# Performance work log

Measured on AMD Instinct MI355X. Metric: run time of the kernel, lower is better.

Reference implementation:

```python
import jax, jax.numpy as jnp
import numpy as np

K, D = 4096, 256
BETA, DECAY, EPS = 0.25, 0.99, 1e-05
B = 32768


def setup_inputs() -> dict:
    key = jax.random.key(0)
    k1, k2, k3, k4 = jax.random.split(key, 4)
    return {
        "z_e": jax.random.normal(k1, (B, D), dtype=jnp.float32),
        "codebook": jax.random.normal(k2, (K, D), dtype=jnp.float32),
        "ema_cluster_size": jax.random.uniform(k3, (K,), dtype=jnp.float32),
        "ema_weight": jax.random.normal(k4, (K, D), dtype=jnp.float32),
    }


def reference(z_e, codebook, ema_cluster_size, ema_weight):
    z_e = z_e.astype(jnp.float32)
    # squared L2 distances: ||z||^2 - 2 z.C^T + ||C||^2  (chunking in torch is
    # purely a memory optimization; math is identical)
    e_norm = jnp.sum(z_e * z_e, axis=1, keepdims=True)            # [B,1]
    c_norm = jnp.sum(codebook * codebook, axis=1)                  # [K]
    dists = e_norm - 2.0 * (z_e @ codebook.T) + c_norm[None, :]    # [B,K]
    idx = jnp.argmin(dists, axis=1)                                # [B] int

    z_q = codebook[idx]                                            # [B,d] gather

    # EMA codebook update (no_grad in torch)
    counts = jnp.zeros((K,), jnp.float32).at[idx].add(1.0)         # bincount
    new_cluster = ema_cluster_size * DECAY + counts * (1.0 - DECAY)
    dw = jnp.zeros((K, D), jnp.float32).at[idx].add(z_e)           # index_add_
    new_ema_weight = ema_weight * DECAY + dw * (1.0 - DECAY)
    n = jnp.sum(new_cluster)
    cluster_size = (new_cluster + EPS) / (n + K * EPS) * n
    new_codebook = new_ema_weight / cluster_size[:, None]

    z_q_ste = z_e + jax.lax.stop_gradient(z_q - z_e)
    commit = BETA * jnp.mean((z_e - z_q) ** 2)
    return (z_q_ste, idx, commit, new_codebook, new_cluster, new_ema_weight)
```

## Files before the change

kernel.cpp:

```cpp
#include <hip/hip_runtime.h>

#define KC 4096
#define DD 256
#define BB 32768
#define P_BETA 0.25f
#define P_DECAY 0.99f
#define P_EPS 1e-5f
#define TAU 0.5f
#define CHUNK 16

typedef __attribute__((ext_vector_type(8))) short bf16x8;
typedef __attribute__((ext_vector_type(4))) float f32x4;

static __device__ __forceinline__ unsigned short f2bf(float f) {
    unsigned int u = __float_as_uint(f);
    unsigned int r = (u + 0x7fffu + ((u >> 16) & 1u)) >> 16;
    return (unsigned short)r;
}
static __device__ __forceinline__ void gload_lds16(const void* g, void* s) {
    __builtin_amdgcn_global_load_lds(
        (const __attribute__((address_space(1))) unsigned int*)g,
        (__attribute__((address_space(3))) unsigned int*)s, 16, 0, 0);
}

#define ZBLK (BB * DD / 4 / 256)
#define CBLK (KC * DD / 4 / 256)
#define EBLK (KC * DD / 4 / 256)
__global__ __launch_bounds__(256) void convert_all_kernel(
    const float* __restrict__ z, const float* __restrict__ cb,
    unsigned short* __restrict__ zb, unsigned short* __restrict__ cbb,
    float* __restrict__ cn, int* __restrict__ cnt,
    const float* __restrict__ ema_w, float* __restrict__ out_emaw) {
    const int b = blockIdx.x;
    if (b < ZBLK) {
        int t = b * 256 + threadIdx.x;
        float4 v = ((const float4*)z)[t];
        *(ushort4*)&zb[(size_t)t * 4] =
            make_ushort4(f2bf(v.x), f2bf(v.y), f2bf(v.z), f2bf(v.w));
    } else if (b < ZBLK + CBLK) {
        int t = (b - ZBLK) * 256 + threadIdx.x;
        int lane = threadIdx.x & 63;
        int row = (b - ZBLK) * 4 + (threadIdx.x >> 6);
        float4 v = ((const float4*)cb)[t];
        *(ushort4*)&cbb[(size_t)t * 4] =
            make_ushort4(f2bf(v.x), f2bf(v.y), f2bf(v.z), f2bf(v.w));
        float s = v.x * v.x + v.y * v.y + v.z * v.z + v.w * v.w;
#pragma unroll
        for (int m = 32; m; m >>= 1) s += __shfl_xor(s, m);
        if (lane == 0) cn[row] = s;
    } else if (b == ZBLK + CBLK) {
        int4* p = (int4*)cnt;
        int4 zv = make_int4(0, 0, 0, 0);
#pragma unroll
        for (int j = 0; j < 4; ++j) p[threadIdx.x * 4 + j] = zv;
    } else {
        int t = (b - ZBLK - CBLK - 1) * 256 + threadIdx.x;
        float4 v = ((const float4*)ema_w)[t];
        ((float4*)out_emaw)[t] =
            make_float4(v.x * P_DECAY, v.y * P_DECAY, v.z * P_DECAY, v.w * P_DECAY);
    }
}

__global__ __launch_bounds__(256, 2) void
mfma_argmin_kernel(const unsigned short* __restrict__ zb,
                   const unsigned short* __restrict__ cbb,
                   const float* __restrict__ cn,
                   float4* __restrict__ cand) {
    __shared__ unsigned short As[128 * 256];
    __shared__ unsigned short Bs[128 * 64];

    const int tid = threadIdx.x;
    const int l = tid & 63, w = tid >> 6;
    const int xcd = blockIdx.x & 7;
    const int half = xcd >> 2;
    const int rb = (blockIdx.x >> 3) * 4 + (xcd & 3);
    const int row0 = rb * 128;
    const int col0 = half * 2048;
    const int wm = w & 1, wn = w >> 1;
    const int m_off = wm * 64, n_off = wn * 64;
    const int lm = l & 15, lq = l >> 4;

    {
        const int lrow = w * 2 + (l >> 5);
        const int coff = ((l & 31) ^ lrow) * 8;
#pragma unroll
        for (int i = 0; i < 16; ++i) {
            gload_lds16(zb + (size_t)(row0 + i * 8 + lrow) * DD + coff,
                        &As[(i * 8 + w * 2) * 256]);
        }
    }

    const int srow = l >> 3;
    const int scol = ((l & 7) ^ srow) * 8;
    const int g0 = w * 4;

    float best[16];
    int bidx[16];
#pragma unroll
    for (int s = 0; s < 16; ++s) { best[s] = 3.4e38f; bidx[s] = 0; }

    for (int kc = 0; kc < 2048; kc += 128) {
        f32x4 acc[4][4];
#pragma unroll
        for (int a = 0; a < 4; ++a)
#pragma unroll
            for (int b = 0; b < 4; ++b) acc[a][b] = (f32x4){0.f, 0.f, 0.f, 0.f};

        for (int dc = 0; dc < 4; ++dc) {
#pragma unroll
            for (int j = 0; j < 4; ++j) {
                const int g = g0 + j;
                const int br = col0 + kc + g * 8 + srow;
                gload_lds16(cbb + (size_t)br * DD + dc * 64 + scol, &Bs[g * 512]);
            }
            __syncthreads();
#pragma unroll
            for (int ks = 0; ks < 2; ++ks) {
                bf16x8 af[4], bfr[4];
                const int cbi = dc * 8 + ks * 4 + lq;
#pragma unroll
                for (int tm = 0; tm < 4; ++tm) {
                    int r = m_off + tm * 16 + lm;
                    af[tm] = *(const bf16x8*)&As[r * 256 + ((cbi ^ (r & 7)) * 8)];
                }
#pragma unroll
                for (int tn = 0; tn < 4; ++tn) {
                    int r = n_off + tn * 16 + lm;
                    bfr[tn] = *(const bf16x8*)&Bs[r * 64 + (((ks * 4 + lq) ^ (r & 7)) * 8)];
                }
#pragma unroll
                for (int tm = 0; tm < 4; ++tm)
#pragma unroll
                    for (int tn = 0; tn < 4; ++tn)
                        acc[tm][tn] = __builtin_amdgcn_mfma_f32_16x16x32_bf16(
                            af[tm], bfr[tn], acc[tm][tn], 0, 0, 0);
            }
            __syncthreads();
        }
#pragma unroll
        for (int tn = 0; tn < 4; ++tn) {
            const int col = col0 + kc + n_off + tn * 16 + lm;
            const float cnv = cn[col];
#pragma unroll
            for (int tm = 0; tm < 4; ++tm)
#pragma unroll
                for (int r = 0; r < 4; ++r) {
                    float dist = fmaf(-2.0f, acc[tm][tn][r], cnv);
                    int s = tm * 4 + r;
                    if (dist < best[s]) { best[s] = dist; bidx[s] = col; }
                }
        }
    }

    float v2[16];
    int i2[16];
#pragma unroll
    for (int s = 0; s < 16; ++s) { v2[s] = 3.4e38f; i2[s] = 0x7fffffff; }
#pragma unroll
    for (int m = 1; m < 16; m <<= 1) {
#pragma unroll
        for (int s = 0; s < 16; ++s) {
            float w1 = __shfl_xor(best[s], m); int j1 = __shfl_xor(bidx[s], m);
            float w2 = __shfl_xor(v2[s], m);   int j2 = __shfl_xor(i2[s], m);
            bool b = (w1 < best[s]) || (w1 == best[s] && j1 < bidx[s]);
            if (b) {
                bool c = (best[s] < w2) || (best[s] == w2 && bidx[s] < j2);
                v2[s] = c ? best[s] : w2; i2[s] = c ? bidx[s] : j2;
                best[s] = w1; bidx[s] = j1;
            } else {
                bool c = (w1 < v2[s]) || (w1 == v2[s] && j1 < i2[s]);
                v2[s] = c ? w1 : v2[s]; i2[s] = c ? j1 : i2[s];
            }
        }
    }

    float4* red = (float4*)As;
    if (lm == 0) {
#pragma unroll
        for (int tm = 0; tm < 4; ++tm)
#pragma unroll
            for (int r = 0; r < 4; ++r) {
                int s = tm * 4 + r;
                int row_local = m_off + tm * 16 + lq * 4 + r;
                red[wn * 128 + row_local] =
                    make_float4(best[s], __int_as_float(bidx[s]), v2[s], __int_as_float(i2[s]));
            }
    }
    __syncthreads();
    if (tid < 128) {
        float4 a = red[tid], b = red[128 + tid];
        float av1 = a.x, av2 = a.z; int ai1 = __float_as_int(a.y), ai2 = __float_as_int(a.w);
        float bv1 = b.x, bv2 = b.z; int bi1 = __float_as_int(b.y), bi2 = __float_as_int(b.w);
        float v1o, v2o; int i1o, i2o;
        bool bb = (bv1 < av1) || (bv1 == av1 && bi1 < ai1);
        if (bb) {
            v1o = bv1; i1o = bi1;
            bool c = (av1 < bv2) || (av1 == bv2 && ai1 < bi2);
            v2o = c ? av1 : bv2; i2o = c ? ai1 : bi2;
        } else {
            v1o = av1; i1o = ai1;
            bool c = (bv1 < av2) || (bv1 == av2 && bi1 < ai2);
            v2o = c ? bv1 : av2; i2o = c ? bi1 : ai2;
        }
        cand[(size_t)half * BB + row0 + tid] =
            make_float4(v1o, __int_as_float(i1o), v2o, __int_as_float(i2o));
    }
}

__global__ __launch_bounds__(256) void merge_refine_kernel(
    const float4* __restrict__ cand, const float* __restrict__ z,
    const float* __restrict__ cb, const float* __restrict__ cn,
    int* __restrict__ idx_i, float* __restrict__ idx_f,
    int* __restrict__ cnt) {
    const int w = threadIdx.x >> 6, l = threadIdx.x & 63;
    const int i = blockIdx.x * 4 + w;
    float4 a = cand[i], b = cand[(size_t)BB + i];
    float av1 = a.x, av2 = a.z; int ai1 = __float_as_int(a.y), ai2 = __float_as_int(a.w);
    float bv1 = b.x, bv2 = b.z; int bi1 = __float_as_int(b.y), bi2 = __float_as_int(b.w);
    float v1o, v2o; int i1o, i2o;
    bool bb = (bv1 < av1) || (bv1 == av1 && bi1 < ai1);
    if (bb) {
        v1o = bv1; i1o = bi1;
        bool c = (av1 < bv2) || (av1 == bv2 && ai1 < bi2);
        v2o = c ? av1 : bv2; i2o = c ? ai1 : bi2;
    } else {
        v1o = av1; i1o = ai1;
        bool c = (bv1 < av2) || (bv1 == av2 && bi1 < ai2);
        v2o = c ? bv1 : av2; i2o = c ? bi1 : ai2;
    }
    int kb = i1o;
    if (v2o - v1o < TAU) {
        float4 zv = ((const float4*)z)[(size_t)i * 64 + l];
        float4 p = ((const float4*)cb)[(size_t)i1o * 64 + l];
        float4 q = ((const float4*)cb)[(size_t)i2o * 64 + l];
        float s1 = zv.x * p.x + zv.y * p.y + zv.z * p.z + zv.w * p.w;
        float s2 = zv.x * q.x + zv.y * q.y + zv.z * q.z + zv.w * q.w;
#pragma unroll
        for (int m = 32; m; m >>= 1) {
            s1 += __shfl_xor(s1, m);
            s2 += __shfl_xor(s2, m);
        }
        float d1 = cn[i1o] - 2.f * s1;
        float d2 = cn[i2o] - 2.f * s2;
        if (d2 < d1 || (d2 == d1 && i2o < i1o)) kb = i2o;
    }
    if (l == 0) {
        idx_i[i] = kb;
        idx_f[i] = (float)kb;
        atomicAdd(&cnt[kb], 1);
    }
}

__global__ __launch_bounds__(256) void prefix_kernel(
    const int* __restrict__ cnt, int* __restrict__ cursor,
    const float* __restrict__ ema_cs, float* __restrict__ out_cluster,
    float* __restrict__ n_ws) {
    __shared__ int ls[257];
    __shared__ float lns[4];
    const int t = threadIdx.x;
    int local[16];
    int s = 0;
    float ns = 0.f;
#pragma unroll
    for (int j = 0; j < 16; ++j) {
        int c = cnt[t * 16 + j];
        local[j] = s; s += c;
        float nc = ema_cs[t * 16 + j] * P_DECAY + (float)c * (1.0f - P_DECAY);
        out_cluster[t * 16 + j] = nc;
        ns += nc;
    }
    ls[t + 1] = s;
#pragma unroll
    for (int m = 32; m; m >>= 1) ns += __shfl_xor(ns, m);
    if ((t & 63) == 0) lns[t >> 6] = ns;
    __syncthreads();
    if (t == 0) {
        ls[0] = 0;
        for (int j = 1; j <= 256; ++j) ls[j] += ls[j - 1];
        *n_ws = lns[0] + lns[1] + lns[2] + lns[3];
    }
    __syncthreads();
    int off = ls[t];
#pragma unroll
    for (int j = 0; j < 16; ++j) cursor[t * 16 + j] = off + local[j];
}

__global__ __launch_bounds__(256) void zq_commit_scatter_kernel(
    const float* __restrict__ z, const float* __restrict__ cb,
    const int* __restrict__ idx_i, float* __restrict__ zq,
    float* __restrict__ commit_parts, int* __restrict__ cursor,
    int* __restrict__ row_of) {
    const int w = threadIdx.x >> 6, l = threadIdx.x & 63;
    const int i = blockIdx.x * 4 + w;
    const int k = idx_i[i];
    float4 zv = ((const float4*)z)[(size_t)i * 64 + l];
    float4 cv = ((const float4*)cb)[(size_t)k * 64 + l];
    ((float4*)zq)[(size_t)i * 64 + l] = cv;
    float dx = zv.x - cv.x, dy = zv.y - cv.y, dz = zv.z - cv.z, dq = zv.w - cv.w;
    float s = dx * dx + dy * dy + dz * dz + dq * dq;
#pragma unroll
    for (int m = 32; m; m >>= 1) s += __shfl_xor(s, m);
    __shared__ float ls[4];
    if (l == 0) {
        ls[w] = s;
        int pos = atomicAdd(&cursor[k], 1);
        row_of[pos] = i | (k << 16);
    }
    __syncthreads();
    if (threadIdx.x == 0) commit_parts[blockIdx.x] = ls[0] + ls[1] + ls[2] + ls[3];
}

__global__ __launch_bounds__(256) void bucket_scatter_kernel(
    const float* __restrict__ z, const int* __restrict__ row_of,
    float* __restrict__ out_emaw, const float* __restrict__ commit_parts,
    float* __restrict__ out_commit) {
    const int t = threadIdx.x;
    if (blockIdx.x == BB / CHUNK) {
        float cs = 0.f;
        for (int j = t; j < BB / 4; j += 256) cs += commit_parts[j];
#pragma unroll
        for (int m = 32; m; m >>= 1) cs += __shfl_xor(cs, m);
        __shared__ float lc[4];
        if ((t & 63) == 0) lc[t >> 6] = cs;
        __syncthreads();
        if (t == 0)
            *out_commit = P_BETA * (lc[0] + lc[1] + lc[2] + lc[3]) / (float)((size_t)BB * DD);
        return;
    }
    __shared__ int pk[CHUNK];
    const int p0 = blockIdx.x * CHUNK;
    if (t < CHUNK) pk[t] = row_of[p0 + t];
    __syncthreads();
    float acc = 0.f;
    int kprev = pk[0] >> 16;
#pragma unroll 4
    for (int j = 0; j < CHUNK; ++j) {
        int p = pk[j];
        int r = p & 0xffff, k = p >> 16;
        if (k != kprev) {
            atomicAdd(&out_emaw[(size_t)kprev * DD + t], acc * (1.0f - P_DECAY));
            acc = 0.f;
            kprev = k;
        }
        acc += z[(size_t)r * DD + t];
    }
    atomicAdd(&out_emaw[(size_t)kprev * DD + t], acc * (1.0f - P_DECAY));
}

__global__ __launch_bounds__(256) void codebook_kernel(
    const float* __restrict__ out_emaw, const float* __restrict__ out_cluster,
    const float* __restrict__ n_ws, float* __restrict__ out_codebook) {
    const int id4 = blockIdx.x * 256 + threadIdx.x;
    const int k = id4 >> 6;
    const float n = *n_ws;
    float4 v = ((const float4*)out_emaw)[id4];
    float cl = out_cluster[k];
    float inv = 1.0f / ((cl + P_EPS) / (n + (float)KC * P_EPS) * n);
    ((float4*)out_codebook)[id4] =
        make_float4(v.x * inv, v.y * inv, v.z * inv, v.w * inv);
}

extern "C" void kernel_launch(void* const* d_in, const int* in_sizes, int n_in,
                              void* d_out, int out_size, void* d_ws, size_t ws_size,
                              hipStream_t stream) {
    const float* z      = (const float*)d_in[0];
    const float* cb     = (const float*)d_in[1];
    const float* ema_cs = (const float*)d_in[2];
    const float* ema_w  = (const float*)d_in[3];

    float4* cand = (float4*)d_ws;
    unsigned short* zb = (unsigned short*)(cand + 2 * (size_t)BB);
    unsigned short* cbb = zb + (size_t)BB * DD;
    float* c_norm = (float*)(cbb + (size_t)KC * DD);
    int* idx_i = (int*)(c_norm + KC);
    int* cnt = idx_i + BB;
    int* cursor = cnt + KC;
    int* row_of = cursor + KC;
    float* commit_parts = (float*)(row_of + BB);
    float* n_ws = commit_parts + BB / 4;

    float* out        = (float*)d_out;
    float* o_zq       = out;
    float* o_idx      = o_zq + (size_t)BB * DD;
    float* o_commit   = o_idx + BB;
    float* o_codebook = o_commit + 1;
    float* o_cluster  = o_codebook + (size_t)KC * DD;
    float* o_emaw     = o_cluster + KC;

    convert_all_kernel<<<ZBLK + CBLK + 1 + EBLK, 256, 0, stream>>>(
        z, cb, zb, cbb, c_norm, cnt, ema_w, o_emaw);
    mfma_argmin_kernel<<<(BB / 128) * 2, 256, 0, stream>>>(zb, cbb, c_norm, cand);
    merge_refine_kernel<<<BB / 4, 256, 0, stream>>>(cand, z, cb, c_norm, idx_i,
                                                    o_idx, cnt);
    prefix_kernel<<<1, 256, 0, stream>>>(cnt, cursor, ema_cs, o_cluster, n_ws);
    zq_commit_scatter_kernel<<<BB / 4, 256, 0, stream>>>(z, cb, idx_i, o_zq,
                                                         commit_parts, cursor, row_of);
    bucket_scatter_kernel<<<BB / CHUNK + 1, 256, 0, stream>>>(
        z, row_of, o_emaw, commit_parts, o_commit);
    codebook_kernel<<<(KC * DD / 4) / 256, 256, 0, stream>>>(
        o_emaw, o_cluster, n_ws, o_codebook);
    (void)in_sizes; (void)n_in; (void)out_size; (void)ws_size;
}
```

Baseline: 228.1 us.

## Fuse merge, zq, commit and direct atomic EMA scatter; drop bucket sort

Merges the candidate-merge/refine, z_q gather, commit partial and EMA weight accumulation into one kernel that adds z rows directly into the EMA weights with per-element atomics. This removes the prefix sort, bucket scatter and separate codebook kernels. The finalize kernel has every block recompute the cluster sum n redundantly. In exchange, 32768×256 float atomics go to global memory, which may contend on popular codes, and the floating-point summation order becomes nondeterministic.

```diff
diff --git a/kernel.cpp b/kernel.cpp
--- a/kernel.cpp
+++ b/kernel.cpp
@@ -7,7 +7,6 @@
 #define P_DECAY 0.99f
 #define P_EPS 1e-5f
 #define TAU 0.5f
-#define CHUNK 16
 
 typedef __attribute__((ext_vector_type(8))) short bf16x8;
 typedef __attribute__((ext_vector_type(4))) float f32x4;
@@ -207,11 +206,12 @@
     }
 }
 
-__global__ __launch_bounds__(256) void merge_refine_kernel(
+__global__ __launch_bounds__(256) void merge_zq_kernel(
     const float4* __restrict__ cand, const float* __restrict__ z,
     const float* __restrict__ cb, const float* __restrict__ cn,
-    int* __restrict__ idx_i, float* __restrict__ idx_f,
-    int* __restrict__ cnt) {
+    float* __restrict__ idx_f, int* __restrict__ cnt,
+    float* __restrict__ zq, float* __restrict__ commit_parts,
+    float* __restrict__ out_emaw) {
     const int w = threadIdx.x >> 6, l = threadIdx.x & 63;
     const int i = blockIdx.x * 4 + w;
     float4 a = cand[i], b = cand[(size_t)BB + i];
@@ -228,10 +228,11 @@
         bool c = (bv1 < av2) || (bv1 == av2 && bi1 < ai2);
         v2o = c ? bv1 : av2; i2o = c ? bi1 : ai2;
     }
+    float4 zv = ((const float4*)z)[(size_t)i * 64 + l];
+    float4 p = ((const float4*)cb)[(size_t)i1o * 64 + l];
     int kb = i1o;
+    float4 cv = p;
     if (v2o - v1o < TAU) {
-        float4 zv = ((const float4*)z)[(size_t)i * 64 + l];
-        float4 p = ((const float4*)cb)[(size_t)i1o * 64 + l];
         float4 q = ((const float4*)cb)[(size_t)i2o * 64 + l];
         float s1 = zv.x * p.x + zv.y * p.y + zv.z * p.z + zv.w * p.w;
         float s2 = zv.x * q.x + zv.y * q.y + zv.z * q.z + zv.w * q.w;
@@ -242,80 +243,36 @@
         }
         float d1 = cn[i1o] - 2.f * s1;
         float d2 = cn[i2o] - 2.f * s2;
-        if (d2 < d1 || (d2 == d1 && i2o < i1o)) kb = i2o;
-    }
-    if (l == 0) {
-        idx_i[i] = kb;
-        idx_f[i] = (float)kb;
-        atomicAdd(&cnt[kb], 1);
-    }
-}
-
-__global__ __launch_bounds__(256) void prefix_kernel(
-    const int* __restrict__ cnt, int* __restrict__ cursor,
-    const float* __restrict__ ema_cs, float* __restrict__ out_cluster,
-    float* __restrict__ n_ws) {
-    __shared__ int ls[257];
-    __shared__ float lns[4];
-    const int t = threadIdx.x;
-    int local[16];
-    int s = 0;
-    float ns = 0.f;
-#pragma unroll
-    for (int j = 0; j < 16; ++j) {
-        int c = cnt[t * 16 + j];
-        local[j] = s; s += c;
-        float nc = ema_cs[t * 16 + j] * P_DECAY + (float)c * (1.0f - P_DECAY);
-        out_cluster[t * 16 + j] = nc;
-        ns += nc;
-    }
-    ls[t + 1] = s;
-#pragma unroll
-    for (int m = 32; m; m >>= 1) ns += __shfl_xor(ns, m);
-    if ((t & 63) == 0) lns[t >> 6] = ns;
-    __syncthreads();
-    if (t == 0) {
-        ls[0] = 0;
-        for (int j = 1; j <= 256; ++j) ls[j] += ls[j - 1];
-        *n_ws = lns[0] + lns[1] + lns[2] + lns[3];
-    }
-    __syncthreads();
-    int off = ls[t];
-#pragma unroll
-    for (int j = 0; j < 16; ++j) cursor[t * 16 + j] = off + local[j];
-}
-
-__global__ __launch_bounds__(256) void zq_commit_scatter_kernel(
-    const float* __restrict__ z, const float* __restrict__ cb,
-    const int* __restrict__ idx_i, float* __restrict__ zq,
-    float* __restrict__ commit_parts, int* __restrict__ cursor,
-    int* __restrict__ row_of) {
-    const int w = threadIdx.x >> 6, l = threadIdx.x & 63;
-    const int i = blockIdx.x * 4 + w;
-    const int k = idx_i[i];
-    float4 zv = ((const float4*)z)[(size_t)i * 64 + l];
-    float4 cv = ((const float4*)cb)[(size_t)k * 64 + l];
+        if (d2 < d1 || (d2 == d1 && i2o < i1o)) { kb = i2o; cv = q; }
+    }
     ((float4*)zq)[(size_t)i * 64 + l] = cv;
     float dx = zv.x - cv.x, dy = zv.y - cv.y, dz = zv.z - cv.z, dq = zv.w - cv.w;
     float s = dx * dx + dy * dy + dz * dz + dq * dq;
 #pragma unroll
     for (int m = 32; m; m >>= 1) s += __shfl_xor(s, m);
+    const float sc = 1.0f - P_DECAY;
+    float* dst = out_emaw + (size_t)kb * DD + l * 4;
+    atomicAdd(dst + 0, zv.x * sc);
+    atomicAdd(dst + 1, zv.y * sc);
+    atomicAdd(dst + 2, zv.z * sc);
+    atomicAdd(dst + 3, zv.w * sc);
     __shared__ float ls[4];
     if (l == 0) {
         ls[w] = s;
-        int pos = atomicAdd(&cursor[k], 1);
-        row_of[pos] = i | (k << 16);
+        idx_f[i] = (float)kb;
+        atomicAdd(&cnt[kb], 1);
     }
     __syncthreads();
     if (threadIdx.x == 0) commit_parts[blockIdx.x] = ls[0] + ls[1] + ls[2] + ls[3];
 }
 
-__global__ __launch_bounds__(256) void bucket_scatter_kernel(
-    const float* __restrict__ z, const int* __restrict__ row_of,
-    float* __restrict__ out_emaw, const float* __restrict__ commit_parts,
+__global__ __launch_bounds__(256) void finalize_kernel(
+    const int* __restrict__ cnt, const float* __restrict__ ema_cs,
+    const float* __restrict__ out_emaw, const float* __restrict__ commit_parts,
+    float* __restrict__ out_cluster, float* __restrict__ out_codebook,
     float* __restrict__ out_commit) {
     const int t = threadIdx.x;
-    if (blockIdx.x == BB / CHUNK) {
+    if (blockIdx.x == KC / 4) {
         float cs = 0.f;
         for (int j = t; j < BB / 4; j += 256) cs += commit_parts[j];
 #pragma unroll
@@ -327,35 +284,26 @@
             *out_commit = P_BETA * (lc[0] + lc[1] + lc[2] + lc[3]) / (float)((size_t)BB * DD);
         return;
     }
-    __shared__ int pk[CHUNK];
-    const int p0 = blockIdx.x * CHUNK;
-    if (t < CHUNK) pk[t] = row_of[p0 + t];
+    float ns = 0.f;
+#pragma unroll
+    for (int j = 0; j < 16; ++j) {
+        int kk = t * 16 + j;
+        float nc = ema_cs[kk] * P_DECAY + (float)cnt[kk] * (1.0f - P_DECAY);
+        ns += nc;
+    }
+#pragma unroll
+    for (int m = 32; m; m >>= 1) ns += __shfl_xor(ns, m);
+    __shared__ float lns[4];
+    if ((t & 63) == 0) lns[t >> 6] = ns;
     __syncthreads();
-    float acc = 0.f;
-    int kprev = pk[0] >> 16;
-#pragma unroll 4
-    for (int j = 0; j < CHUNK; ++j) {
-        int p = pk[j];
-        int r = p & 0xffff, k = p >> 16;
-        if (k != kprev) {
-            atomicAdd(&out_emaw[(size_t)kprev * DD + t], acc * (1.0f - P_DECAY));
-            acc = 0.f;
-            kprev = k;
-        }
-        acc += z[(size_t)r * DD + t];
-    }
-    atomicAdd(&out_emaw[(size_t)kprev * DD + t], acc * (1.0f - P_DECAY));
-}
-
-__global__ __launch_bounds__(256) void codebook_kernel(
-    const float* __restrict__ out_emaw, const float* __restrict__ out_cluster,
-    const float* __restrict__ n_ws, float* __restrict__ out_codebook) {
-    const int id4 = blockIdx.x * 256 + threadIdx.x;
+    const float n = lns[0] + lns[1] + lns[2] + lns[3];
+
+    const int id4 = blockIdx.x * 256 + t;
     const int k = id4 >> 6;
-    const float n = *n_ws;
+    float cl = ema_cs[k] * P_DECAY + (float)cnt[k] * (1.0f - P_DECAY);
+    if ((t & 63) == 0) out_cluster[k] = cl;
+    float inv = 1.0f / ((cl + P_EPS) / (n + (float)KC * P_EPS) * n);
     float4 v = ((const float4*)out_emaw)[id4];
-    float cl = out_cluster[k];
-    float inv = 1.0f / ((cl + P_EPS) / (n + (float)KC * P_EPS) * n);
     ((float4*)out_codebook)[id4] =
         make_float4(v.x * inv, v.y * inv, v.z * inv, v.w * inv);
 }
@@ -372,12 +320,8 @@
     unsigned short* zb = (unsigned short*)(cand + 2 * (size_t)BB);
     unsigned short* cbb = zb + (size_t)BB * DD;
     float* c_norm = (float*)(cbb + (size_t)KC * DD);
-    int* idx_i = (int*)(c_norm + KC);
-    int* cnt = idx_i + BB;
-    int* cursor = cnt + KC;
-    int* row_of = cursor + KC;
-    float* commit_parts = (float*)(row_of + BB);
-    float* n_ws = commit_parts + BB / 4;
+    int* cnt = (int*)(c_norm + KC);
+    float* commit_parts = (float*)(cnt + KC);
 
     float* out        = (float*)d_out;
     float* o_zq       = out;
@@ -390,14 +334,10 @@
     convert_all_kernel<<<ZBLK + CBLK + 1 + EBLK, 256, 0, stream>>>(
         z, cb, zb, cbb, c_norm, cnt, ema_w, o_emaw);
     mfma_argmin_kernel<<<(BB / 128) * 2, 256, 0, stream>>>(zb, cbb, c_norm, cand);
-    merge_refine_kernel<<<BB / 4, 256, 0, stream>>>(cand, z, cb, c_norm, idx_i,
-                                                    o_idx, cnt);
-    prefix_kernel<<<1, 256, 0, stream>>>(cnt, cursor, ema_cs, o_cluster, n_ws);
-    zq_commit_scatter_kernel<<<BB / 4, 256, 0, stream>>>(z, cb, idx_i, o_zq,
-                                                         commit_parts, cursor, row_of);
-    bucket_scatter_kernel<<<BB / CHUNK + 1, 256, 0, stream>>>(
-        z, row_of, o_emaw, commit_parts, o_commit);
-    codebook_kernel<<<(KC * DD / 4) / 256, 256, 0, stream>>>(
-        o_emaw, o_cluster, n_ws, o_codebook);
+    merge_zq_kernel<<<BB / 4, 256, 0, stream>>>(cand, z, cb, c_norm, o_idx, cnt,
+                                                o_zq, commit_parts, o_emaw);
+    finalize_kernel<<<KC / 4 + 1, 256, 0, stream>>>(cnt, ema_cs, o_emaw,
+                                                    commit_parts, o_cluster,
+                                                    o_codebook, o_commit);
     (void)in_sizes; (void)n_in; (void)out_size; (void)ws_size;
 }
```

Result: slower. 351.2 us (+53.9%).
